# Optimization experiments

Hardware: AMD Instinct MI355X
Metric: run time of the kernel (lower is better)

Reference implementation:

```python
import jax, jax.numpy as jnp
import numpy as np
from jax import lax

# ---- config (matches DecodePredictions init kwargs) ----
MAX_PER_CLASS = 100
MAX_TOTAL = 100
IOU_THRESH = 0.5
SCORE_THRESH = 0.05
NUM_CLASSES = 80
K_CAND = 512  # per-class candidate pool kept before NMS (bounds the O(K^2) IoU work)
BOX_VARIANCE = np.array([0.1, 0.1, 0.2, 0.2], np.float32)


def generate_anchors(height, width):
    """RetinaNet anchors (keras.io AnchorBox): FPN levels 3-7, 3 ratios x 3 scales, [cx,cy,w,h] in pixels."""
    ratios = [0.5, 1.0, 2.0]
    scales = [2 ** 0.0, 2 ** (1.0 / 3.0), 2 ** (2.0 / 3.0)]
    all_anchors = []
    for level in range(3, 8):
        stride = 2 ** level
        area = float((2 ** (level + 2)) ** 2)  # 32^2 .. 512^2
        dims = []
        for r in ratios:
            ah = np.sqrt(area / r)
            aw = area / ah
            for s in scales:
                dims.append([s * aw, s * ah])
        dims = np.asarray(dims, np.float32)  # [9, 2] = (w, h)
        fh = int(np.ceil(height / stride))
        fw = int(np.ceil(width / stride))
        rx = (np.arange(fw, dtype=np.float32) + 0.5) * stride
        ry = (np.arange(fh, dtype=np.float32) + 0.5) * stride
        cx, cy = np.meshgrid(rx, ry)
        centers = np.stack([cx, cy], -1)[:, :, None, :].repeat(9, axis=2)  # [fh,fw,9,2]
        d = np.broadcast_to(dims, (fh, fw, 9, 2))
        all_anchors.append(np.concatenate([centers, d], -1).reshape(-1, 4).astype(np.float32))
    return jnp.asarray(np.concatenate(all_anchors, 0))  # [N, 4]


def _pairwise_iou(b):
    # Generic TF NMS IoU formula treating coords as [y1,x1,y2,x2] (module feeds cx,cy,w,h -- replicated faithfully).
    y1, x1, y2, x2 = b[:, 0], b[:, 1], b[:, 2], b[:, 3]
    area = jnp.maximum(y2 - y1, 0.0) * jnp.maximum(x2 - x1, 0.0)
    ih = jnp.maximum(jnp.minimum(y2[:, None], y2[None, :]) - jnp.maximum(y1[:, None], y1[None, :]), 0.0)
    iw = jnp.maximum(jnp.minimum(x2[:, None], x2[None, :]) - jnp.maximum(x1[:, None], x1[None, :]), 0.0)
    inter = ih * iw
    union = area[:, None] + area[None, :] - inter
    return jnp.where(union > 0.0, inter / union, 0.0)


def _nms_single_class(boxes, scores):  # boxes [N,4], scores [N]
    top_s, idx = lax.top_k(scores, K_CAND)          # sort-by-score candidate pool
    top_b = boxes[idx]                               # [K,4]
    keep0 = top_s > SCORE_THRESH                     # score_threshold filter
    iou = _pairwise_iou(top_b)                       # [K,K]
    rng = jnp.arange(K_CAND)

    def body(i, keep):
        sup = (iou[i] > IOU_THRESH) & (rng > i)      # boxes ranked below i suppressed by i
        return jnp.where(keep[i], keep & ~sup, keep)

    keep = lax.fori_loop(0, K_CAND, body, keep0)
    kept_s = jnp.where(keep, top_s, 0.0)
    sel_s, sel = lax.top_k(kept_s, MAX_PER_CLASS)    # max_output_size_per_class
    return top_b[sel], sel_s                         # [P,4], [P]


def _combine(cls_boxes, cls_scores):  # [C,P,4], [C,P] -> combined top MAX_TOTAL for one image
    C, P = cls_scores.shape
    flat_s = cls_scores.reshape(-1)
    flat_b = cls_boxes.reshape(-1, 4)
    flat_c = jnp.repeat(jnp.arange(C, dtype=jnp.float32), P)
    top_s, idx = lax.top_k(flat_s, MAX_TOTAL)
    valid = (top_s > 0.0)
    vf = valid.astype(flat_b.dtype)
    boxes = jnp.clip(flat_b[idx], 0.0, 1.0) * vf[:, None]  # clip_boxes=True, zero-pad invalid
    scores = top_s * vf
    classes = jnp.where(valid, flat_c[idx], 0.0)
    return boxes, scores, classes, valid.sum().astype(jnp.int32)


def _forward(inputs, predictions):
    H, W = inputs.shape[1], inputs.shape[2]
    anchors = generate_anchors(float(H), float(W))            # [N,4] cx,cy,w,h
    cls_scores = jax.nn.sigmoid(predictions[..., :-4])        # [B,N,C]
    box_pred = predictions[..., -4:] * jnp.asarray(BOX_VARIANCE)
    xy = box_pred[..., :2] * anchors[..., 2:] + anchors[..., :2]
    wh = jnp.exp(box_pred[..., 2:]) * anchors[..., 2:]
    boxes = jnp.concatenate([xy, wh], -1)                     # [B,N,4] decoded

    per_class = jax.vmap(jax.vmap(_nms_single_class, in_axes=(None, 1)), in_axes=(0, 0))
    cb, cs = per_class(boxes, cls_scores)                     # [B,C,P,4], [B,C,P]
    return jax.vmap(_combine)(cb, cs)                         # boxes, scores, classes, valid


def setup_inputs() -> dict:
    key = jax.random.key(0)
    k1, k2 = jax.random.split(key)
    inputs = jax.random.uniform(k1, (4, 640, 640, 3), jnp.float32)
    predictions = jax.random.normal(k2, (4, 76725, NUM_CLASSES + 4), jnp.float32)
    return {"inputs": inputs, "predictions": predictions}


def reference(inputs, predictions):
    return _forward(inputs, predictions)
```

## Files before the change

### kernel.cpp

```cpp
#include <hip/hip_runtime.h>
#include <cmath>

#define NA 76725
#define NCLS 80
#define NB 4
#define KC 512
#define MPC 100
#define MT 100
#define TT 128
#define LROW 85
#define NTILE 600
#define PADN 76800
#define CAP 4096
#define NSLOT 1200
#define SLOT 16
#define SPLIT 4
#define THRESH_LOGIT 2.0f

struct Dims { float d[5 * 9 * 2]; };


__device__ __forceinline__ unsigned keyof(float x) {
    unsigned u = __float_as_uint(x);
    return u ^ ((u & 0x80000000u) ? 0xFFFFFFFFu : 0x80000000u);
}
__device__ __forceinline__ float unkey(unsigned k) {
    unsigned u = (k & 0x80000000u) ? (k ^ 0x80000000u) : ~k;
    return __uint_as_float(u);
}
__device__ __forceinline__ float sigmoidf_dev(float x) {
    if (x >= 0.f) return 1.f / (1.f + expf(-x));
    float e = expf(x);
    return e / (1.f + e);
}
__device__ __forceinline__ unsigned long long compose(unsigned key, int a) {
    return ((unsigned long long)key << 32) | (unsigned long long)(0xFFFFFFFFu - (unsigned)a);
}

__device__ __forceinline__ float4 decode_box(float4 p, int a, const Dims& dims) {
    const int base[5] = {0, 57600, 72000, 75600, 76500};
    const int fw[5] = {80, 40, 20, 10, 5};
    const float strd[5] = {8.f, 16.f, 32.f, 64.f, 128.f};
    int l;
    if (a < 57600) l = 0;
    else if (a < 72000) l = 1;
    else if (a < 75600) l = 2;
    else if (a < 76500) l = 3;
    else l = 4;
    int i = a - base[l];
    int cell = i / 9, k = i - cell * 9;
    int x = cell % fw[l], y = cell / fw[l];
    float cx = ((float)x + 0.5f) * strd[l];
    float cy = ((float)y + 0.5f) * strd[l];
    float aw = dims.d[(l * 9 + k) * 2 + 0];
    float ah = dims.d[(l * 9 + k) * 2 + 1];
    float bx = __fmul_rn(p.x, 0.1f), by = __fmul_rn(p.y, 0.1f);
    float bw = __fmul_rn(p.z, 0.2f), bh = __fmul_rn(p.w, 0.2f);
    float4 o;
    o.x = __fadd_rn(__fmul_rn(bx, aw), cx);
    o.y = __fadd_rn(__fmul_rn(by, ah), cy);
    o.z = __fmul_rn(expf(bw), aw);
    o.w = __fmul_rn(expf(bh), ah);
    return o;
}


__global__ __launch_bounds__(256) void scan_decode_kernel(const float* __restrict__ pred,
                                                          unsigned long long* __restrict__ candbuf,
                                                          int* __restrict__ counts2,
                                                          float4* __restrict__ boxes, Dims dims) {
    __shared__ float tile[TT * LROW];
    const int blk = blockIdx.x;
    const int b = blk / NTILE, tix = blk - b * NTILE;
    const int t0 = tix * TT;
    int nrow = NA - t0; if (nrow > TT) nrow = TT;

    const float4* src = reinterpret_cast<const float4*>(pred + ((size_t)b * NA + t0) * 84);
    const int nv = nrow * 21;
    for (int i = threadIdx.x; i < nv; i += 256) {
        float4 v = src[i];
        const int row = i / 21, fo = (i - row * 21) * 4;
        float* dst = &tile[row * LROW + fo];
        dst[0] = v.x; dst[1] = v.y; dst[2] = v.z; dst[3] = v.w;
    }
    __syncthreads();

    const int wv = threadIdx.x >> 6;
    const int lane = threadIdx.x & 63;
    const int chalf = wv >> 1;
    const int rhalf = wv & 1;
    const int r = rhalf * 64 + lane;
    const bool valid = r < nrow;
    const int a = t0 + r;
    const int c0 = chalf * 40;
    const int slot = tix * 2 + rhalf;
    const float* rowp = &tile[r * LROW];

    int mycnt = 0;
    for (int j = 0; j < 40; ++j) {
        const float x = valid ? rowp[c0 + j] : -1e30f;
        const bool hit = x > THRESH_LOGIT;
        const unsigned long long m = __ballot(hit);
        const int cnt = __popcll(m);
        if (lane == j) mycnt = cnt;
        if (hit) {
            const int rank = __popcll(m & ((1ull << lane) - 1ull));
            if (rank < SLOT) {
                const int col = b * NCLS + c0 + j;
                candbuf[((size_t)col * NSLOT + slot) * SLOT + rank] = compose(keyof(x), a);
            }
        }
    }
    if (lane < 40) {
        const int col = b * NCLS + c0 + lane;
        counts2[(size_t)slot * (NB * NCLS) + col] = mycnt;
    }

    if (wv < 2 && valid) {
        float4 p4;
        p4.x = rowp[80]; p4.y = rowp[81]; p4.z = rowp[82]; p4.w = rowp[83];
        boxes[(size_t)b * NA + a] = decode_box(p4, a, dims);
    }
}


__device__ __forceinline__ void find_bin(int* hist, int bins, int remaining,
                                         int* sh3, int* wsum) {
    const int tid = threadIdx.x;
    const int lane = tid & 63, wv = tid >> 6;
    const int nit = (bins + 1023) >> 10;
    int lsum = 0;
    for (int q = 0; q < nit; ++q) {
        int rr = tid * nit + q;
        if (rr < bins) lsum += hist[bins - 1 - rr];
    }
    int acc = lsum;
    #pragma unroll
    for (int off = 1; off < 64; off <<= 1) {
        int x = __shfl_up(acc, off);
        if (lane >= off) acc += x;
    }
    if (lane == 63) wsum[wv] = acc;
    __syncthreads();
    int base = 0;
    for (int w = 0; w < wv; ++w) base += wsum[w];
    int run = base + acc - lsum;
    for (int q = 0; q < nit; ++q) {
        int rr = tid * nit + q;
        if (rr < bins) {
            int h = hist[bins - 1 - rr];
            if (run < remaining && remaining <= run + h) { sh3[0] = bins - 1 - rr; sh3[1] = run; sh3[2] = h; }
            run += h;
        }
    }
    __syncthreads();
}


__global__ __launch_bounds__(1024) void topk2_kernel(const float* __restrict__ pred,
                                                     const unsigned long long* __restrict__ candbuf,
                                                     const int* __restrict__ counts2,
                                                     int* __restrict__ top_idx,
                                                     float* __restrict__ top_score) {
    const int col = blockIdx.x;
    const int b = col / NCLS, cc = col - b * NCLS;
    const int tid = threadIdx.x;
    const int lane = tid & 63, wv = tid >> 6;

    __shared__ int hist[4096];
    __shared__ unsigned long long cand[CAP];
    __shared__ unsigned long long buf[KC];
    __shared__ int scnt[NSLOT];
    __shared__ int spfx[NSLOT];
    __shared__ int sh3[3];
    __shared__ int wsum[16];
    __shared__ int gcount, eqtaken, totsh, ovfsh;
    __shared__ int wcnt[16];

    for (int i = tid; i < NSLOT; i += 1024)
        scnt[i] = counts2[(size_t)i * (NB * NCLS) + col];
    if (tid == 0) { totsh = 0; ovfsh = 0; }
    __syncthreads();

    const int e0 = 2 * tid, e1 = 2 * tid + 1;
    int c0s = 0, c1s = 0;
    if (e0 < NSLOT) { c0s = scnt[e0]; c1s = scnt[e1]; }
    if (c0s > SLOT || c1s > SLOT) ovfsh = 1;
    const int pair = c0s + c1s;
    int acc = pair;
    #pragma unroll
    for (int off = 1; off < 64; off <<= 1) {
        int x = __shfl_up(acc, off);
        if (lane >= off) acc += x;
    }
    if (lane == 63) wsum[wv] = acc;
    __syncthreads();
    int base = 0;
    for (int w = 0; w < wv; ++w) base += wsum[w];
    if (e0 < NSLOT) {
        const int excl = base + acc - pair;
        spfx[e0] = excl;
        spfx[e1] = excl + c0s;
    }
    if (tid == 1023) totsh = base + acc;
    __syncthreads();

    const int tot = totsh;
    const bool fastok = (!ovfsh) && tot >= KC && tot <= CAP;
    int nc = -1;

    if (fastok) {
        for (int e = tid; e < NSLOT; e += 1024) {
            const int ce = scnt[e];
            const int p = spfx[e];
            const unsigned long long* sp = candbuf + ((size_t)col * NSLOT + e) * SLOT;
            for (int q = 0; q < ce; ++q) cand[p + q] = sp[q];
        }
        nc = tot;
        __syncthreads();
    } else {
        const float* colp = pred + (size_t)b * NA * 84 + cc;
        for (int i = tid; i < 4096; i += 1024) hist[i] = 0;
        __syncthreads();
        for (int a = tid; a < NA; a += 1024)
            atomicAdd(&hist[keyof(colp[(size_t)a * 84]) >> 20], 1);
        __syncthreads();
        find_bin(hist, 4096, KC, sh3, wsum);
        const int bsel = sh3[0], above = sh3[1], ceq1 = sh3[2];
        const int ncand = above + ceq1;

        if (ncand <= CAP) {
            const unsigned fk = ((unsigned)bsel) << 20;
            if (tid == 0) gcount = 0;
            __syncthreads();
            for (int a = tid; a < NA; a += 1024) {
                unsigned k = keyof(colp[(size_t)a * 84]);
                if (k >= fk) { int p = atomicAdd(&gcount, 1); cand[p] = compose(k, a); }
            }
            __syncthreads();
            nc = gcount;
        } else {
            unsigned prefix = ((unsigned)bsel) << 20;
            int remaining = KC - above;

            for (int i = tid; i < 4096; i += 1024) hist[i] = 0;
            __syncthreads();
            for (int a = tid; a < NA; a += 1024) {
                unsigned k = keyof(colp[(size_t)a * 84]);
                if ((k & 0xFFF00000u) == prefix) atomicAdd(&hist[(k >> 8) & 4095], 1);
            }
            __syncthreads();
            find_bin(hist, 4096, remaining, sh3, wsum);
            prefix |= ((unsigned)sh3[0]) << 8;
            remaining -= sh3[1];

            if (tid < 256) hist[tid] = 0;
            __syncthreads();
            for (int a = tid; a < NA; a += 1024) {
                unsigned k = keyof(colp[(size_t)a * 84]);
                if ((k & 0xFFFFFF00u) == prefix) atomicAdd(&hist[k & 255], 1);
            }
            __syncthreads();
            find_bin(hist, 256, remaining, sh3, wsum);
            prefix |= (unsigned)sh3[0];
            remaining -= sh3[1];

            const unsigned K = prefix;
            const int cgt = KC - remaining;
            const int need = remaining;
            if (tid == 0) { gcount = 0; eqtaken = 0; }
            __syncthreads();
            for (int bs = 0; bs < PADN; bs += 1024) {
                int a = bs + tid;
                unsigned key = (a < NA) ? keyof(colp[(size_t)a * 84]) : 0u;
                if (a < NA && key > K) {
                    int p = atomicAdd(&gcount, 1);
                    buf[p] = compose(key, a);
                }
                bool eq = (key == K) && (a < NA);
                unsigned long long m = __ballot(eq);
                if (lane == 0) wcnt[wv] = __popcll(m);
                __syncthreads();
                int off = eqtaken;
                for (int w = 0; w < wv; ++w) off += wcnt[w];
                int rank = off + __popcll(m & ((1ull << lane) - 1ull));
                if (eq && rank < need)
                    buf[cgt + rank] = compose(K, a);
                __syncthreads();
                if (tid == 0) {
                    int s = 0;
                    for (int w = 0; w < 16; ++w) s += wcnt[w];
                    eqtaken += s;
                }
                __syncthreads();
            }
            nc = -1;
        }
    }

    if (nc >= 0) {
        unsigned long long cpre = 0ull;
        int rem512 = KC;
        for (int pass = 0; pass < 8; ++pass) {
            const int shift = 56 - 8 * pass;
            const unsigned long long mdone = pass ? ((~0ull) << (shift + 8)) : 0ull;
            if (tid < 256) hist[tid] = 0;
            __syncthreads();
            for (int t = tid; t < nc; t += 1024) {
                unsigned long long k = cand[t];
                if ((k & mdone) == cpre) atomicAdd(&hist[(int)((k >> shift) & 255)], 1);
            }
            __syncthreads();
            find_bin(hist, 256, rem512, sh3, wsum);
            cpre |= ((unsigned long long)(unsigned)sh3[0]) << shift;
            rem512 -= sh3[1];
            __syncthreads();
        }
        if (tid == 0) gcount = 0;
        __syncthreads();
        for (int t = tid; t < nc; t += 1024) {
            unsigned long long k = cand[t];
            if (k >= cpre) { int p = atomicAdd(&gcount, 1); buf[p] = k; }
        }
        __syncthreads();
    }

    for (int k2 = 2; k2 <= KC; k2 <<= 1) {
        for (int j = k2 >> 1; j > 0; j >>= 1) {
            __syncthreads();
            if (tid < KC) {
                int i = tid, ixj = i ^ j;
                if (ixj > i) {
                    unsigned long long A = buf[i], B = buf[ixj];
                    bool up = (i & k2) == 0;
                    if (up ? (A < B) : (A > B)) { buf[i] = B; buf[ixj] = A; }
                }
            }
        }
    }
    __syncthreads();
    if (tid < KC) {
        unsigned long long v = buf[tid];
        unsigned key = (unsigned)(v >> 32);
        int a = (int)(0xFFFFFFFFu - (unsigned)(v & 0xFFFFFFFFu));
        top_idx[col * KC + tid] = a;
        top_score[col * KC + tid] = sigmoidf_dev(unkey(key));
    }
}


__global__ __launch_bounds__(256) void nms_build_kernel(const float4* __restrict__ boxes,
                                                        const int* __restrict__ top_idx,
                                                        unsigned long long* __restrict__ maskbuf) {
    const int blk = blockIdx.x;
    const int col = blk / SPLIT, part = blk - col * SPLIT;
    const int b = col / NCLS;
    const int tid = threadIdx.x, wave = tid >> 6, lane = tid & 63;
    __shared__ float y1[KC], x1[KC], y2[KC], x2[KC], ar[KC];

    for (int t = tid; t < KC; t += 256) {
        int idx = top_idx[col * KC + t];
        float4 bx = boxes[(size_t)b * NA + idx];
        y1[t] = bx.x; x1[t] = bx.y; y2[t] = bx.z; x2[t] = bx.w;
        ar[t] = __fmul_rn(fmaxf(__fsub_rn(bx.z, bx.x), 0.f),
                          fmaxf(__fsub_rn(bx.w, bx.y), 0.f));
    }
    __syncthreads();

    float jy1[8], jx1[8], jy2[8], jx2[8], jar[8];
    #pragma unroll
    for (int w = 0; w < 8; ++w) {
        int j = (w << 6) + lane;
        jy1[w] = y1[j]; jx1[w] = x1[j]; jy2[w] = y2[j]; jx2[w] = x2[j]; jar[w] = ar[j];
    }

    for (int k = 0; k < 32; ++k) {
        const int i = part + SPLIT * (wave + 4 * k);
        const float iy1 = y1[i], ix1 = x1[i], iy2 = y2[i], ix2 = x2[i], iar = ar[i];
        unsigned long long row[8];
        #pragma unroll
        for (int w = 0; w < 8; ++w) {
            unsigned long long m = 0ull;
            if (((w << 6) + 63) > i) {
                const int j = (w << 6) + lane;
                float ih = fmaxf(__fsub_rn(fminf(iy2, jy2[w]), fmaxf(iy1, jy1[w])), 0.f);
                float iw = fmaxf(__fsub_rn(fminf(ix2, jx2[w]), fmaxf(ix1, jx1[w])), 0.f);
                float inter = __fmul_rn(ih, iw);
                float uni = __fsub_rn(__fadd_rn(iar, jar[w]), inter);
                m = __ballot((uni > 0.f) && (inter > __fmul_rn(0.5f, uni)) && (j > i));
            }
            row[w] = m;
        }
        unsigned long long v = row[0];
        v = (lane == 1) ? row[1] : v;
        v = (lane == 2) ? row[2] : v;
        v = (lane == 3) ? row[3] : v;
        v = (lane == 4) ? row[4] : v;
        v = (lane == 5) ? row[5] : v;
        v = (lane == 6) ? row[6] : v;
        v = (lane == 7) ? row[7] : v;
        if (lane < 8) maskbuf[((size_t)col * KC + i) * 8 + lane] = v;
    }
}


__global__ __launch_bounds__(256) void nms_resolve_kernel(const float4* __restrict__ boxes,
                                                          const int* __restrict__ top_idx,
                                                          const float* __restrict__ top_score,
                                                          const unsigned long long* __restrict__ maskbuf,
                                                          float4* __restrict__ col_boxes,
                                                          float* __restrict__ col_scores) {
    const int col = blockIdx.x, b = col / NCLS;
    const int tid = threadIdx.x, lane = tid & 63;
    __shared__ unsigned long long mask[KC * 8];
    __shared__ float sc[KC];
    __shared__ unsigned char rowany[KC];
    __shared__ unsigned long long keep0w[8], keepw[8];
    __shared__ int wordpfx[9];
    __shared__ int sel[MPC];

    {
        const unsigned long long* src = maskbuf + (size_t)col * KC * 8;
        const int r0 = tid * 2;
        unsigned long long any0 = 0ull, any1 = 0ull;
        #pragma unroll
        for (int q = 0; q < 8; ++q) { unsigned long long v = src[r0 * 8 + q]; mask[r0 * 8 + q] = v; any0 |= v; }
        #pragma unroll
        for (int q = 0; q < 8; ++q) { unsigned long long v = src[(r0 + 1) * 8 + q]; mask[(r0 + 1) * 8 + q] = v; any1 |= v; }
        rowany[r0] = any0 ? 1 : 0;
        rowany[r0 + 1] = any1 ? 1 : 0;
    }
    for (int t = tid; t < KC; t += 256) {
        float s = top_score[col * KC + t];
        sc[t] = s;
        unsigned long long m = __ballot(s > 0.05f);
        if (lane == 0) keep0w[t >> 6] = m;
    }
    __syncthreads();

    if (tid == 0) {
        unsigned long long rem[8] = {0, 0, 0, 0, 0, 0, 0, 0};
        #pragma unroll
        for (int W = 0; W < 8; ++W) {
            const unsigned long long kw = keep0w[W];
            for (int t = 0; t < 64; ++t) {
                const int i = (W << 6) + t;
                bool alive = ((kw >> t) & 1ull) && !((rem[W] >> t) & 1ull);
                if (alive && rowany[i]) {
                    const unsigned long long* row = &mask[i * 8];
                    #pragma unroll
                    for (int w2 = W; w2 < 8; ++w2) rem[w2] |= row[w2];
                }
            }
        }
        int s = 0;
        #pragma unroll
        for (int w = 0; w < 8; ++w) {
            keepw[w] = keep0w[w] & ~rem[w];
            wordpfx[w] = s;
            s += __popcll(keepw[w]);
        }
        wordpfx[8] = s;
    }
    __syncthreads();

    const int nkept = wordpfx[8];
    for (int t = tid; t < KC; t += 256) {
        const unsigned long long w = keepw[t >> 6];
        const int l = t & 63;
        const bool kp = (w >> l) & 1ull;
        const int kb = wordpfx[t >> 6] + __popcll(w & ((1ull << l) - 1ull));
        if (kp) {
            if (kb < MPC) sel[kb] = t;
        } else {
            const int nb = t - kb;
            if (nkept + nb < MPC) sel[nkept + nb] = t;
        }
    }
    __syncthreads();
    if (tid < MPC) {
        int t = sel[tid];
        bool kp = (keepw[t >> 6] >> (t & 63)) & 1ull;
        col_scores[col * MPC + tid] = kp ? sc[t] : 0.f;
        int idx = top_idx[col * KC + t];
        col_boxes[col * MPC + tid] = boxes[(size_t)b * NA + idx];
    }
}


__global__ __launch_bounds__(256) void combine_kernel(const float4* __restrict__ col_boxes,
                                                      const float* __restrict__ col_scores,
                                                      float* __restrict__ out) {
    const int b = blockIdx.x, tid = threadIdx.x;
    const int wv = tid >> 6, lane = tid & 63;
    __shared__ int hist[256];
    __shared__ int partial[256];
    __shared__ unsigned long long cand[128];
    __shared__ int sh3[3];
    __shared__ int gcnt, eqtaken;
    __shared__ int wcnt[4];

    unsigned sck[32];
    #pragma unroll
    for (int q = 0; q < 32; ++q) {
        const bool ok = (q < 31) || (tid < 64);
        sck[q] = ok ? __float_as_uint(col_scores[b * NCLS * MPC + (q << 8) + tid]) : 0u;
    }

    unsigned prefix = 0;
    int remaining = MT, ceq = 0;
    #pragma unroll 1
    for (int pass = 0; pass < 4; ++pass) {
        const int shift = 24 - 8 * pass;
        const unsigned mdone = pass ? (0xFFFFFFFFu << (shift + 8)) : 0u;
        hist[tid] = 0;
        __syncthreads();
        #pragma unroll
        for (int q = 0; q < 32; ++q) {
            const bool ok = (q < 31) || (tid < 64);
            if (ok && (sck[q] & mdone) == prefix)
                atomicAdd(&hist[(sck[q] >> shift) & 255], 1);
        }
        __syncthreads();
        int lsum = hist[255 - tid];
        partial[tid] = lsum;
        __syncthreads();
        int acc = lsum;
        for (int off = 1; off < 256; off <<= 1) {
            int x = (tid >= off) ? partial[tid - off] : 0;
            __syncthreads();
            acc += x;
            partial[tid] = acc;
            __syncthreads();
        }
        int run = acc - lsum;
        if (run < remaining && remaining <= run + lsum) { sh3[0] = 255 - tid; sh3[1] = run; sh3[2] = lsum; }
        __syncthreads();
        prefix |= ((unsigned)sh3[0]) << shift;
        remaining -= sh3[1];
        ceq = sh3[2];
        __syncthreads();
    }
    const unsigned S = prefix;
    const int cgt = MT - remaining;

    if (tid == 0) { gcnt = 0; eqtaken = 0; }
    if (tid < 128) cand[tid] = 0ull;
    __syncthreads();
    #pragma unroll
    for (int q = 0; q < 32; ++q) {
        const bool ok = (q < 31) || (tid < 64);
        if (ok && sck[q] > S) {
            int p = atomicAdd(&gcnt, 1);
            int t = (q << 8) + tid;
            cand[p] = ((unsigned long long)sck[q] << 32) |
                      (unsigned long long)(0xFFFFFFFFu - (unsigned)t);
        }
    }
    __syncthreads();

    if (ceq == remaining) {
        #pragma unroll
        for (int q = 0; q < 32; ++q) {
            const bool ok = (q < 31) || (tid < 64);
            if (ok && sck[q] == S) {
                int p = atomicAdd(&eqtaken, 1);
                int t = (q << 8) + tid;
                cand[cgt + p] = ((unsigned long long)S << 32) |
                                (unsigned long long)(0xFFFFFFFFu - (unsigned)t);
            }
        }
        __syncthreads();
    } else {
        #pragma unroll 1
        for (int q = 0; q < 32; ++q) {
            const bool ok = (q < 31) || (tid < 64);
            const bool eq = ok && (sck[q] == S);
            unsigned long long m = __ballot(eq);
            if (lane == 0) wcnt[wv] = __popcll(m);
            __syncthreads();
            int off = eqtaken;
            for (int w = 0; w < wv; ++w) off += wcnt[w];
            int rank = off + __popcll(m & ((1ull << lane) - 1ull));
            if (eq && rank < remaining) {
                int t = (q << 8) + tid;
                cand[cgt + rank] = ((unsigned long long)S << 32) |
                                   (unsigned long long)(0xFFFFFFFFu - (unsigned)t);
            }
            __syncthreads();
            if (tid == 0) eqtaken += wcnt[0] + wcnt[1] + wcnt[2] + wcnt[3];
            __syncthreads();
        }
    }

    for (int k2 = 2; k2 <= 128; k2 <<= 1) {
        for (int j = k2 >> 1; j > 0; j >>= 1) {
            __syncthreads();
            if (tid < 128) {
                int i = tid, ixj = i ^ j;
                if (ixj > i) {
                    unsigned long long A = cand[i], B = cand[ixj];
                    bool up = (i & k2) == 0;
                    if (up ? (A < B) : (A > B)) { cand[i] = B; cand[ixj] = A; }
                }
            }
        }
    }
    __syncthreads();
    if (tid == 0) gcnt = 0;
    __syncthreads();
    if (tid < MT) {
        unsigned long long v = cand[tid];
        float s = __uint_as_float((unsigned)(v >> 32));
        int f = (int)(0xFFFFFFFFu - (unsigned)(v & 0xFFFFFFFFu));
        bool valid = (s > 0.f);
        int cl = 0, p = 0;
        float4 bx = make_float4(0.f, 0.f, 0.f, 0.f);
        if (valid) {
            cl = f / MPC;
            p = f - cl * MPC;
            float4 raw = col_boxes[((size_t)b * NCLS + cl) * MPC + p];
            bx.x = fminf(fmaxf(raw.x, 0.f), 1.f);
            bx.y = fminf(fmaxf(raw.y, 0.f), 1.f);
            bx.z = fminf(fmaxf(raw.z, 0.f), 1.f);
            bx.w = fminf(fmaxf(raw.w, 0.f), 1.f);
            atomicAdd(&gcnt, 1);
        }
        int o = b * MT + tid;
        out[o * 4 + 0] = bx.x;
        out[o * 4 + 1] = bx.y;
        out[o * 4 + 2] = bx.z;
        out[o * 4 + 3] = bx.w;
        out[NB * MT * 4 + o] = valid ? s : 0.f;
        out[NB * MT * 5 + o] = valid ? (float)cl : 0.f;
    }
    __syncthreads();
    if (tid == 0) out[NB * MT * 6 + b] = (float)gcnt;
}


extern "C" void kernel_launch(void* const* d_in, const int* in_sizes, int n_in,
                              void* d_out, int out_size, void* d_ws, size_t ws_size,
                              hipStream_t stream) {
    const float* pred = (const float*)d_in[1];
    float* out = (float*)d_out;
    char* ws = (char*)d_ws;

    Dims dims;
    const double ratios[3] = {0.5, 1.0, 2.0};
    for (int l = 0; l < 5; ++l) {
        double side = (double)(1 << (l + 5));
        double area = side * side;
        for (int ri = 0; ri < 3; ++ri) {
            double ah = sqrt(area / ratios[ri]);
            double aw = area / ah;
            for (int si = 0; si < 3; ++si) {
                double s = pow(2.0, (double)si / 3.0);
                dims.d[(l * 9 + ri * 3 + si) * 2 + 0] = (float)(s * aw);
                dims.d[(l * 9 + ri * 3 + si) * 2 + 1] = (float)(s * ah);
            }
        }
    }

    const size_t SZ_BOXES = (size_t)NB * NA * 16;
    const size_t SZ_CAND  = (size_t)NB * NCLS * NSLOT * SLOT * 8;
    const size_t SZ_CNT   = (size_t)NSLOT * NB * NCLS * 4;
    const size_t SZ_TOPI  = (size_t)NB * NCLS * KC * 4;
    const size_t SZ_CB    = (size_t)NB * NCLS * MPC * 16;

    float4*             boxes      = (float4*)(ws);
    unsigned long long* candbuf    = (unsigned long long*)(ws + SZ_BOXES);
    int*                counts2    = (int*)(ws + SZ_BOXES + SZ_CAND);
    int*                top_idx    = (int*)(ws + SZ_BOXES + SZ_CAND + SZ_CNT);
    float*              top_score  = (float*)(ws + SZ_BOXES + SZ_CAND + SZ_CNT + SZ_TOPI);
    float4*             col_boxes  = (float4*)(ws + SZ_BOXES + SZ_CAND + SZ_CNT + 2 * SZ_TOPI);
    float*              col_scores = (float*)(ws + SZ_BOXES + SZ_CAND + SZ_CNT + 2 * SZ_TOPI + SZ_CB);
    unsigned long long* maskbuf    = (unsigned long long*)(ws + SZ_BOXES);

    scan_decode_kernel<<<NB * NTILE, 256, 0, stream>>>(pred, candbuf, counts2, boxes, dims);
    topk2_kernel<<<NB * NCLS, 1024, 0, stream>>>(pred, candbuf, counts2, top_idx, top_score);
    nms_build_kernel<<<NB * NCLS * SPLIT, 256, 0, stream>>>(boxes, top_idx, maskbuf);
    nms_resolve_kernel<<<NB * NCLS, 256, 0, stream>>>(boxes, top_idx, top_score, maskbuf, col_boxes, col_scores);
    combine_kernel<<<NB, 256, 0, stream>>>(col_boxes, col_scores, out);
}
```

Before: 367.6 us.

## Fuse NMS build/resolve, decode boxes lazily, and make candidate slots column-contiguous

Removes the full box-decode pass from the scan kernel. Boxes are now decoded only for the 512 top-k candidates inside a single fused NMS kernel, which builds the IoU mask in shared memory instead of writing and re-reading a global mask buffer. The sequential single-thread suppression loop becomes a wave-parallel version using shuffles. The scan tile shrinks to 64 rows with one slot per tile, and counts/candidates are laid out per column so topk can read them contiguously. The trade-off is less parallelism in the NMS stage, with one block per column instead of four build blocks.

```diff
diff --git a/kernel.cpp b/kernel.cpp
--- a/kernel.cpp
+++ b/kernel.cpp
@@ -7,14 +7,14 @@
 #define KC 512
 #define MPC 100
 #define MT 100
-#define TT 128
+#define TT 64
 #define LROW 85
-#define NTILE 600
+#define NTILE 1199
+#define NSLOTP 1199
+#define NSLOTPAD 1216
 #define PADN 76800
 #define CAP 4096
-#define NSLOT 1200
 #define SLOT 16
-#define SPLIT 4
 #define THRESH_LOGIT 2.0f
 
 struct Dims { float d[5 * 9 * 2]; };
@@ -65,10 +65,9 @@
 }
 
 
-__global__ __launch_bounds__(256) void scan_decode_kernel(const float* __restrict__ pred,
-                                                          unsigned long long* __restrict__ candbuf,
-                                                          int* __restrict__ counts2,
-                                                          float4* __restrict__ boxes, Dims dims) {
+__global__ __launch_bounds__(256) void scan_kernel(const float* __restrict__ pred,
+                                                   unsigned long long* __restrict__ candbuf,
+                                                   int* __restrict__ counts2) {
     __shared__ float tile[TT * LROW];
     const int blk = blockIdx.x;
     const int b = blk / NTILE, tix = blk - b * NTILE;
@@ -85,42 +84,29 @@
     }
     __syncthreads();
 
-    const int wv = threadIdx.x >> 6;
-    const int lane = threadIdx.x & 63;
-    const int chalf = wv >> 1;
-    const int rhalf = wv & 1;
-    const int r = rhalf * 64 + lane;
-    const bool valid = r < nrow;
-    const int a = t0 + r;
-    const int c0 = chalf * 40;
-    const int slot = tix * 2 + rhalf;
-    const float* rowp = &tile[r * LROW];
+    const int wv = threadIdx.x >> 6, lane = threadIdx.x & 63;
+    const int c0 = wv * 20;
+    const bool valid = lane < nrow;
+    const int a = t0 + lane;
+    const float* rowp = &tile[lane * LROW];
 
     int mycnt = 0;
-    for (int j = 0; j < 40; ++j) {
+    #pragma unroll
+    for (int j = 0; j < 20; ++j) {
         const float x = valid ? rowp[c0 + j] : -1e30f;
         const bool hit = x > THRESH_LOGIT;
         const unsigned long long m = __ballot(hit);
-        const int cnt = __popcll(m);
-        if (lane == j) mycnt = cnt;
+        if (lane == j) mycnt = __popcll(m);
         if (hit) {
             const int rank = __popcll(m & ((1ull << lane) - 1ull));
             if (rank < SLOT) {
                 const int col = b * NCLS + c0 + j;
-                candbuf[((size_t)col * NSLOT + slot) * SLOT + rank] = compose(keyof(x), a);
-            }
-        }
-    }
-    if (lane < 40) {
-        const int col = b * NCLS + c0 + lane;
-        counts2[(size_t)slot * (NB * NCLS) + col] = mycnt;
-    }
-
-    if (wv < 2 && valid) {
-        float4 p4;
-        p4.x = rowp[80]; p4.y = rowp[81]; p4.z = rowp[82]; p4.w = rowp[83];
-        boxes[(size_t)b * NA + a] = decode_box(p4, a, dims);
-    }
+                candbuf[((size_t)col * NSLOTP + tix) * SLOT + rank] = compose(keyof(x), a);
+            }
+        }
+    }
+    if (lane < 20)
+        counts2[(size_t)(b * NCLS + c0 + lane) * NSLOTP + tix] = mycnt;
 }
 
 
@@ -170,21 +156,22 @@
     __shared__ int hist[4096];
     __shared__ unsigned long long cand[CAP];
     __shared__ unsigned long long buf[KC];
-    __shared__ int scnt[NSLOT];
-    __shared__ int spfx[NSLOT];
+    __shared__ int scnt[NSLOTPAD];
+    __shared__ int spfx[NSLOTPAD];
     __shared__ int sh3[3];
     __shared__ int wsum[16];
     __shared__ int gcount, eqtaken, totsh, ovfsh;
     __shared__ int wcnt[16];
 
-    for (int i = tid; i < NSLOT; i += 1024)
-        scnt[i] = counts2[(size_t)i * (NB * NCLS) + col];
+    for (int i = tid; i < NSLOTP; i += 1024)
+        scnt[i] = counts2[(size_t)col * NSLOTP + i];
+    if (tid < NSLOTPAD - NSLOTP) scnt[NSLOTP + tid] = 0;
     if (tid == 0) { totsh = 0; ovfsh = 0; }
     __syncthreads();
 
     const int e0 = 2 * tid, e1 = 2 * tid + 1;
     int c0s = 0, c1s = 0;
-    if (e0 < NSLOT) { c0s = scnt[e0]; c1s = scnt[e1]; }
+    if (e0 < NSLOTPAD) { c0s = scnt[e0]; c1s = scnt[e1]; }
     if (c0s > SLOT || c1s > SLOT) ovfsh = 1;
     const int pair = c0s + c1s;
     int acc = pair;
@@ -197,7 +184,7 @@
     __syncthreads();
     int base = 0;
     for (int w = 0; w < wv; ++w) base += wsum[w];
-    if (e0 < NSLOT) {
+    if (e0 < NSLOTPAD) {
         const int excl = base + acc - pair;
         spfx[e0] = excl;
         spfx[e1] = excl + c0s;
@@ -210,11 +197,11 @@
     int nc = -1;
 
     if (fastok) {
-        for (int e = tid; e < NSLOT; e += 1024) {
-            const int ce = scnt[e];
-            const int p = spfx[e];
-            const unsigned long long* sp = candbuf + ((size_t)col * NSLOT + e) * SLOT;
-            for (int q = 0; q < ce; ++q) cand[p + q] = sp[q];
+        const unsigned long long* src = candbuf + (size_t)col * NSLOTP * SLOT;
+        for (int i = tid; i < NSLOTP * SLOT; i += 1024) {
+            const int e = i >> 4, q = i & (SLOT - 1);
+            const unsigned long long v = src[i];
+            if (q < scnt[e]) cand[spfx[e] + q] = v;
         }
         nc = tot;
         __syncthreads();
@@ -349,21 +336,30 @@
 }
 
 
-__global__ __launch_bounds__(256) void nms_build_kernel(const float4* __restrict__ boxes,
-                                                        const int* __restrict__ top_idx,
-                                                        unsigned long long* __restrict__ maskbuf) {
-    const int blk = blockIdx.x;
-    const int col = blk / SPLIT, part = blk - col * SPLIT;
-    const int b = col / NCLS;
-    const int tid = threadIdx.x, wave = tid >> 6, lane = tid & 63;
-    __shared__ float y1[KC], x1[KC], y2[KC], x2[KC], ar[KC];
+__global__ __launch_bounds__(256) void nms_kernel(const float* __restrict__ pred,
+                                                  const int* __restrict__ top_idx,
+                                                  const float* __restrict__ top_score,
+                                                  float4* __restrict__ col_boxes,
+                                                  float* __restrict__ col_scores, Dims dims) {
+    const int col = blockIdx.x, b = col / NCLS;
+    const int tid = threadIdx.x, wv = tid >> 6, lane = tid & 63;
+    __shared__ unsigned long long mask[KC * 8];
+    __shared__ float y1[KC], x1[KC], y2[KC], x2[KC], ar[KC], sc[KC];
+    __shared__ unsigned long long keep0w[8], keepw[8];
+    __shared__ int wordpfx[9];
+    __shared__ int sel[MPC];
 
     for (int t = tid; t < KC; t += 256) {
-        int idx = top_idx[col * KC + t];
-        float4 bx = boxes[(size_t)b * NA + idx];
+        const int idx = top_idx[col * KC + t];
+        const float4 p4 = *reinterpret_cast<const float4*>(pred + ((size_t)b * NA + idx) * 84 + 80);
+        const float4 bx = decode_box(p4, idx, dims);
         y1[t] = bx.x; x1[t] = bx.y; y2[t] = bx.z; x2[t] = bx.w;
         ar[t] = __fmul_rn(fmaxf(__fsub_rn(bx.z, bx.x), 0.f),
                           fmaxf(__fsub_rn(bx.w, bx.y), 0.f));
+        const float s = top_score[col * KC + t];
+        sc[t] = s;
+        const unsigned long long m = __ballot(s > 0.05f);
+        if (lane == 0) keep0w[t >> 6] = m;
     }
     __syncthreads();
 
@@ -374,8 +370,8 @@
         jy1[w] = y1[j]; jx1[w] = x1[j]; jy2[w] = y2[j]; jx2[w] = x2[j]; jar[w] = ar[j];
     }
 
-    for (int k = 0; k < 32; ++k) {
-        const int i = part + SPLIT * (wave + 4 * k);
+    for (int k = 0; k < 128; ++k) {
+        const int i = wv + 4 * k;
         const float iy1 = y1[i], ix1 = x1[i], iy2 = y2[i], ix2 = x2[i], iar = ar[i];
         unsigned long long row[8];
         #pragma unroll
@@ -399,67 +395,33 @@
         v = (lane == 5) ? row[5] : v;
         v = (lane == 6) ? row[6] : v;
         v = (lane == 7) ? row[7] : v;
-        if (lane < 8) maskbuf[((size_t)col * KC + i) * 8 + lane] = v;
-    }
-}
-
-
-__global__ __launch_bounds__(256) void nms_resolve_kernel(const float4* __restrict__ boxes,
-                                                          const int* __restrict__ top_idx,
-                                                          const float* __restrict__ top_score,
-                                                          const unsigned long long* __restrict__ maskbuf,
-                                                          float4* __restrict__ col_boxes,
-                                                          float* __restrict__ col_scores) {
-    const int col = blockIdx.x, b = col / NCLS;
-    const int tid = threadIdx.x, lane = tid & 63;
-    __shared__ unsigned long long mask[KC * 8];
-    __shared__ float sc[KC];
-    __shared__ unsigned char rowany[KC];
-    __shared__ unsigned long long keep0w[8], keepw[8];
-    __shared__ int wordpfx[9];
-    __shared__ int sel[MPC];
-
-    {
-        const unsigned long long* src = maskbuf + (size_t)col * KC * 8;
-        const int r0 = tid * 2;
-        unsigned long long any0 = 0ull, any1 = 0ull;
-        #pragma unroll
-        for (int q = 0; q < 8; ++q) { unsigned long long v = src[r0 * 8 + q]; mask[r0 * 8 + q] = v; any0 |= v; }
-        #pragma unroll
-        for (int q = 0; q < 8; ++q) { unsigned long long v = src[(r0 + 1) * 8 + q]; mask[(r0 + 1) * 8 + q] = v; any1 |= v; }
-        rowany[r0] = any0 ? 1 : 0;
-        rowany[r0 + 1] = any1 ? 1 : 0;
-    }
-    for (int t = tid; t < KC; t += 256) {
-        float s = top_score[col * KC + t];
-        sc[t] = s;
-        unsigned long long m = __ballot(s > 0.05f);
-        if (lane == 0) keep0w[t >> 6] = m;
-    }
-    __syncthreads();
-
+        if (lane < 8) mask[i * 8 + lane] = v;
+    }
+    __syncthreads();
+
+    if (wv == 0) {
+        const int w8 = lane & 7;
+        const unsigned long long kww = keep0w[w8];
+        unsigned long long remw = 0ull;
+        for (int ib = 0; ib < KC; ib += 8) {
+            unsigned long long rows[8];
+            #pragma unroll
+            for (int u = 0; u < 8; ++u) rows[u] = mask[(ib + u) * 8 + w8];
+            #pragma unroll
+            for (int u = 0; u < 8; ++u) {
+                const int i = ib + u, W = i >> 6, t = i & 63;
+                const unsigned long long remW = __shfl(remw, W);
+                const unsigned long long kwW = __shfl(kww, W);
+                if (((kwW >> t) & 1ull) && !((remW >> t) & 1ull)) remw |= rows[u];
+            }
+        }
+        if (lane < 8) keepw[w8] = kww & ~remw;
+    }
+    __syncthreads();
     if (tid == 0) {
-        unsigned long long rem[8] = {0, 0, 0, 0, 0, 0, 0, 0};
-        #pragma unroll
-        for (int W = 0; W < 8; ++W) {
-            const unsigned long long kw = keep0w[W];
-            for (int t = 0; t < 64; ++t) {
-                const int i = (W << 6) + t;
-                bool alive = ((kw >> t) & 1ull) && !((rem[W] >> t) & 1ull);
-                if (alive && rowany[i]) {
-                    const unsigned long long* row = &mask[i * 8];
-                    #pragma unroll
-                    for (int w2 = W; w2 < 8; ++w2) rem[w2] |= row[w2];
-                }
-            }
-        }
         int s = 0;
         #pragma unroll
-        for (int w = 0; w < 8; ++w) {
-            keepw[w] = keep0w[w] & ~rem[w];
-            wordpfx[w] = s;
-            s += __popcll(keepw[w]);
-        }
+        for (int w = 0; w < 8; ++w) { wordpfx[w] = s; s += __popcll(keepw[w]); }
         wordpfx[8] = s;
     }
     __syncthreads();
@@ -482,8 +444,7 @@
         int t = sel[tid];
         bool kp = (keepw[t >> 6] >> (t & 63)) & 1ull;
         col_scores[col * MPC + tid] = kp ? sc[t] : 0.f;
-        int idx = top_idx[col * KC + t];
-        col_boxes[col * MPC + tid] = boxes[(size_t)b * NA + idx];
+        col_boxes[col * MPC + tid] = make_float4(y1[t], x1[t], y2[t], x2[t]);
     }
 }
 
@@ -662,24 +623,20 @@
         }
     }
 
-    const size_t SZ_BOXES = (size_t)NB * NA * 16;
-    const size_t SZ_CAND  = (size_t)NB * NCLS * NSLOT * SLOT * 8;
-    const size_t SZ_CNT   = (size_t)NSLOT * NB * NCLS * 4;
-    const size_t SZ_TOPI  = (size_t)NB * NCLS * KC * 4;
-    const size_t SZ_CB    = (size_t)NB * NCLS * MPC * 16;
-
-    float4*             boxes      = (float4*)(ws);
-    unsigned long long* candbuf    = (unsigned long long*)(ws + SZ_BOXES);
-    int*                counts2    = (int*)(ws + SZ_BOXES + SZ_CAND);
-    int*                top_idx    = (int*)(ws + SZ_BOXES + SZ_CAND + SZ_CNT);
-    float*              top_score  = (float*)(ws + SZ_BOXES + SZ_CAND + SZ_CNT + SZ_TOPI);
-    float4*             col_boxes  = (float4*)(ws + SZ_BOXES + SZ_CAND + SZ_CNT + 2 * SZ_TOPI);
-    float*              col_scores = (float*)(ws + SZ_BOXES + SZ_CAND + SZ_CNT + 2 * SZ_TOPI + SZ_CB);
-    unsigned long long* maskbuf    = (unsigned long long*)(ws + SZ_BOXES);
-
-    scan_decode_kernel<<<NB * NTILE, 256, 0, stream>>>(pred, candbuf, counts2, boxes, dims);
+    const size_t SZ_CAND = (size_t)NB * NCLS * NSLOTP * SLOT * 8;
+    const size_t SZ_CNT  = (size_t)NB * NCLS * NSLOTP * 4;
+    const size_t SZ_TOPI = (size_t)NB * NCLS * KC * 4;
+    const size_t SZ_CB   = (size_t)NB * NCLS * MPC * 16;
+
+    unsigned long long* candbuf    = (unsigned long long*)(ws);
+    int*                counts2    = (int*)(ws + SZ_CAND);
+    int*                top_idx    = (int*)(ws + SZ_CAND + SZ_CNT);
+    float*              top_score  = (float*)(ws + SZ_CAND + SZ_CNT + SZ_TOPI);
+    float4*             col_boxes  = (float4*)(ws + SZ_CAND + SZ_CNT + 2 * SZ_TOPI);
+    float*              col_scores = (float*)(ws + SZ_CAND + SZ_CNT + 2 * SZ_TOPI + SZ_CB);
+
+    scan_kernel<<<NB * NTILE, 256, 0, stream>>>(pred, candbuf, counts2);
     topk2_kernel<<<NB * NCLS, 1024, 0, stream>>>(pred, candbuf, counts2, top_idx, top_score);
-    nms_build_kernel<<<NB * NCLS * SPLIT, 256, 0, stream>>>(boxes, top_idx, maskbuf);
-    nms_resolve_kernel<<<NB * NCLS, 256, 0, stream>>>(boxes, top_idx, top_score, maskbuf, col_boxes, col_scores);
+    nms_kernel<<<NB * NCLS, 256, 0, stream>>>(pred, top_idx, top_score, col_boxes, col_scores, dims);
     combine_kernel<<<NB, 256, 0, stream>>>(col_boxes, col_scores, out);
 }
```

Result: slower. 383.9 us (+4.4%).
